# Optimization experiments

Measured on AMD Instinct MI355X. Metric: run time of the kernel, lower is better.

Reference implementation:

```python
import jax, jax.numpy as jnp
import numpy as np

B, NF, HS, S = 4, 5, 512, 1024  # batch, face strips, face side dims (L=9, S=2*HS)


def _wrap_prev(region, x, j, i, w, rev=False):
    # neighbour on previous face strip, wrapping face 0 -> face 4
    vm = x[:, :4, j, i]
    vw = x[:, 4, j, i]
    if rev:
        vm = jnp.flip(vm, -1)
        vw = jnp.flip(vw, -1)
    return jnp.concatenate([(vw - region[:, 0])[:, None] * w,
                            (vm - region[:, 1:]) * w], axis=1)


def _wrap_next(region, x, j, i, w, rev=False):
    # neighbour on next face strip, wrapping face 4 -> face 0
    vm = x[:, 1:, j, i]
    vw = x[:, 0, j, i]
    if rev:
        vm = jnp.flip(vm, -1)
        vw = jnp.flip(vw, -1)
    return jnp.concatenate([(vm - region[:, :4]) * w,
                            (vw - region[:, 4])[:, None] * w], axis=1)


def _gradient(x, poles, wi, we, wcn, wne, wnne, wnw, wnww, wwe, wsw, wsse, wse, wcs):
    Bx, Fx, HS, S = x.shape
    out = jnp.zeros((Bx, 4, Fx, HS, S), x.dtype)

    def put(o, rows, cols, comps):
        return o.at[:, :, :, rows, cols].set(jnp.stack(comps, axis=1))

    # inner grid
    ii = x[:, :, 1:HS-1, 1:S-1]
    comps = [
        (x[:, :, :HS-2, :S-2] - ii) * wi[0],
        (x[:, :, 2:HS, 2:S] - ii) * wi[1],
        (x[:, :, :HS-2, 1:S-1] - ii) * wi[2] + (x[:, :, 1:HS-1, 2:S] - ii) * wi[3],
        (x[:, :, 1:HS-1, :S-2] - ii) * wi[4] + (x[:, :, 2:HS, 1:S-1] - ii) * wi[5],
    ]
    out = put(out, slice(1, HS-1), slice(1, S-1), comps)

    # east edge
    ei = x[:, :, 0, 1:HS]
    comps = [
        _wrap_prev(ei, x, HS-1, slice(HS, S-1), we[0]),
        (x[:, :, 1, 2:HS+1] - ei) * we[1],
        _wrap_prev(ei, x, HS-1, slice(HS+1, S), we[2]) + (x[:, :, 0, 2:HS+1] - ei) * we[3],
        (x[:, :, 0, 0:HS-1] - ei) * we[4] + (x[:, :, 1, 1:HS] - ei) * we[5],
    ]
    out = put(out, 0, slice(1, HS), comps)

    # cn corner
    ci = x[:, :, 0, HS]
    comps = [
        _wrap_prev(ci, x, HS-1, S-1, wcn[0]),
        (x[:, :, 1, HS+1] - ci) * wcn[1],
        (x[:, :, 0, HS+1] - ci) * wcn[2],
        (x[:, :, 0, HS-1] - ci) * wcn[3] + (x[:, :, 1, HS] - ci) * wcn[4],
    ]
    out = put(out, 0, HS, comps)

    # ne edge
    ni = x[:, :, 0, HS+1:S-1]
    comps = [
        _wrap_prev(ni, x, slice(1, HS-1), S-1, wne[0], rev=True) + _wrap_prev(ni, x, slice(2, HS), S-1, wne[1], rev=True),
        (x[:, :, 1, HS+2:S] - ni) * wne[2] + (x[:, :, 1, HS+1:S-1] - ni) * wne[3],
        (x[:, :, 0, HS+2:S] - ni) * wne[4],
        (x[:, :, 0, HS:S-2] - ni) * wne[5],
    ]
    out = put(out, 0, slice(HS+1, S-1), comps)

    # nne corner (north pole neighbour)
    qi = x[:, :, 0, S-1]
    comps = [
        _wrap_prev(qi, x, 0, S-1, wnne[0]) + _wrap_prev(qi, x, 1, S-1, wnne[1]),
        _wrap_next(qi, x, 0, S-1, wnne[2]) + (x[:, :, 1, S-1] - qi) * wnne[3],
        (poles[:, 1] - qi) * wnne[4],
        (x[:, :, 0, S-2] - qi) * wnne[5],
    ]
    out = put(out, 0, S-1, comps)

    # nw edge
    vi = x[:, :, 1:HS-1, S-1]
    comps = [
        (x[:, :, 0:HS-2, S-2] - vi) * wnw[0],
        _wrap_next(vi, x, 0, slice(HS+1, S-1), wnw[1], rev=True),
        (x[:, :, 0:HS-2, S-1] - vi) * wnw[2] + _wrap_next(vi, x, 0, slice(HS+2, S), wnw[3], rev=True),
        (x[:, :, 1:HS-1, S-2] - vi) * wnw[4] + (x[:, :, 2:HS, S-1] - vi) * wnw[5],
    ]
    out = put(out, slice(1, HS-1), S-1, comps)

    # nww corner
    gi = x[:, :, HS-1, S-1]
    comps = [
        (x[:, :, HS-2, S-2] - gi) * wnww[0],
        _wrap_next(gi, x, 0, HS, wnww[1]),
        (x[:, :, HS-2, S-1] - gi) * wnww[2] + _wrap_next(gi, x, 0, HS+1, wnww[3]),
        (x[:, :, HS-1, S-2] - gi) * wnww[4] + _wrap_next(gi, x, 0, HS-1, wnww[5]),
    ]
    out = put(out, HS-1, S-1, comps)

    # west edge
    ui = x[:, :, HS-1, HS:S-1]
    comps = [
        (x[:, :, HS-2, HS-1:S-2] - ui) * wwe[0],
        _wrap_next(ui, x, 0, slice(1, HS), wwe[1]),
        (x[:, :, HS-2, HS:S-1] - ui) * wwe[2] + (x[:, :, HS-1, HS+1:S] - ui) * wwe[3],
        (x[:, :, HS-1, HS-1:S-2] - ui) * wwe[4] + _wrap_next(ui, x, 0, slice(0, HS-1), wwe[5]),
    ]
    out = put(out, HS-1, slice(HS, S-1), comps)

    # sw edge
    si = x[:, :, HS-1, 1:HS]
    comps = [
        (x[:, :, HS-2, 0:HS-1] - si) * wsw[0],
        _wrap_next(si, x, slice(0, HS-1), 0, wsw[1], rev=True),
        (x[:, :, HS-2, 1:HS] - si) * wsw[2] + (x[:, :, HS-1, 2:HS+1] - si) * wsw[3],
        (x[:, :, HS-1, 0:HS-1] - si) * wsw[4] + _wrap_next(si, x, slice(1, HS), 0, wsw[5], rev=True),
    ]
    out = put(out, HS-1, slice(1, HS), comps)

    # sse corner (south pole neighbour)
    pi = x[:, :, HS-1, 0]
    comps = [
        _wrap_prev(pi, x, HS-1, 0, wsse[0]),
        _wrap_next(pi, x, HS-1, 0, wsse[1]),
        (x[:, :, HS-2, 0] - pi) * wsse[2] + (x[:, :, HS-1, 1] - pi) * wsse[3],
        (poles[:, 0] - pi) * wsse[4],
    ]
    out = put(out, HS-1, 0, comps)

    # se edge
    ri = x[:, :, 1:HS-1, 0]
    comps = [
        _wrap_prev(ri, x, HS-1, slice(2, HS), wse[0], rev=True) + _wrap_prev(ri, x, HS-1, slice(1, HS-1), wse[1], rev=True),
        (x[:, :, 1:HS-1, 1] - ri) * wse[2] + (x[:, :, 2:HS, 1] - ri) * wse[3],
        (x[:, :, 0:HS-2, 0] - ri) * wse[4],
        (x[:, :, 2:HS, 0] - ri) * wse[5],
    ]
    out = put(out, slice(1, HS-1), 0, comps)

    # cs corner
    di = x[:, :, 0, 0]
    comps = [
        _wrap_prev(di, x, HS-1, HS-1, wcs[0]),
        (x[:, :, 1, 1] - di) * wcs[1],
        _wrap_prev(di, x, HS-1, HS, wcs[2]) + (x[:, :, 0, 1] - di) * wcs[3],
        (x[:, :, 1, 0] - di) * wcs[4],
    ]
    out = put(out, 0, 0, comps)
    return out


def setup_inputs() -> dict:
    key = jax.random.key(0)
    ks = jax.random.split(key, 14)
    rn = lambda k, s: jax.random.normal(k, s, dtype=jnp.float32)
    return {
        "x": rn(ks[0], (B, NF, HS, S)),
        "poles": rn(ks[1], (B, 2, 1)),
        "w_inner": rn(ks[2], (6, HS-2, S-2)),
        "w_east": rn(ks[3], (6, HS-1)),
        "w_cn": rn(ks[4], (5,)),
        "w_ne": rn(ks[5], (6, HS-2)),
        "w_nne": rn(ks[6], (6,)),
        "w_nw": rn(ks[7], (6, HS-2)),
        "w_nww": rn(ks[8], (6,)),
        "w_west": rn(ks[9], (6, HS-1)),
        "w_sw": rn(ks[10], (6, HS-1)),
        "w_sse": rn(ks[11], (5,)),
        "w_se": rn(ks[12], (6, HS-2)),
        "w_cs": rn(ks[13], (5,)),
    }


def reference(x, poles, w_inner, w_east, w_cn, w_ne, w_nne, w_nw, w_nww, w_west, w_sw, w_sse, w_se, w_cs):
    # output: [B, 4, 5, HS, S] weighted neighbour-difference stencil components
    return _gradient(x, poles, w_inner, w_east, w_cn, w_ne, w_nne, w_nw, w_nww,
                     w_west, w_sw, w_sse, w_se, w_cs)
```

## Files before the change

kernel.cpp:

```cpp
#include <hip/hip_runtime.h>

#define Bc  4
#define NFc 5
#define HSc 512
#define Sc  1024
#define WSr (Sc - 2)
#define WSp ((HSc - 2) * WSr)

typedef float f4 __attribute__((ext_vector_type(4)));

static __device__ __forceinline__ f4 load4u(const float* p) {
    f4 r;
    __builtin_memcpy(&r, p, 16);
    return r;
}

static __device__ __forceinline__ void inner_scalar(
    const float* __restrict__ xf, const float* __restrict__ wi,
    int j, int i, float cc, float* c)
{
    const size_t wb = (size_t)(j - 1) * WSr + (i - 1);
    const float w0 = wi[wb];
    const float w1 = wi[wb + WSp];
    const float w2 = wi[wb + 2 * (size_t)WSp];
    const float w3 = wi[wb + 3 * (size_t)WSp];
    const float w4 = wi[wb + 4 * (size_t)WSp];
    const float w5 = wi[wb + 5 * (size_t)WSp];
    c[0] = (xf[(size_t)(j - 1) * Sc + (i - 1)] - cc) * w0;
    c[1] = (xf[(size_t)(j + 1) * Sc + (i + 1)] - cc) * w1;
    c[2] = (xf[(size_t)(j - 1) * Sc + i] - cc) * w2
         + (xf[(size_t)j * Sc + (i + 1)] - cc) * w3;
    c[3] = (xf[(size_t)j * Sc + (i - 1)] - cc) * w4
         + (xf[(size_t)(j + 1) * Sc + i] - cc) * w5;
}

__global__ __launch_bounds__(256) void icograd_bulk(
    const float* __restrict__ x, const float* __restrict__ wi,
    const float* __restrict__ wnw, const float* __restrict__ wse,
    float* __restrict__ out)
{
    const int t  = threadIdx.x;
    const int j  = blockIdx.x + 1;
    const int bf = blockIdx.y;
    const int b  = bf / NFc;
    const int f  = bf % NFc;

    const size_t xb = (size_t)b * (NFc * HSc * Sc);
    const float* xf = x + xb + (size_t)f * (HSc * Sc);
    const float* rm = xf + (size_t)(j - 1) * Sc;
    const float* rc = xf + (size_t)j * Sc;
    const float* rp = xf + (size_t)(j + 1) * Sc;
    const int i0 = t * 4;

    float c0[4], c1[4], c2[4], c3[4];

    if (t >= 1 && t <= 254) {
        const f4 xm = *(const f4*)(rm + i0);
        const f4 xc = *(const f4*)(rc + i0);
        const f4 xp = *(const f4*)(rp + i0);
        const float xml = rm[i0 - 1];
        const float xcl = rc[i0 - 1];
        const float xcr = rc[i0 + 4];
        const float xpr = rp[i0 + 4];

        const float* wrow = wi + (size_t)(j - 1) * WSr + (i0 - 1);
        const f4 w0 = load4u(wrow);
        const f4 w1 = load4u(wrow + (size_t)WSp);
        const f4 w2 = load4u(wrow + 2 * (size_t)WSp);
        const f4 w3 = load4u(wrow + 3 * (size_t)WSp);
        const f4 w4 = load4u(wrow + 4 * (size_t)WSp);
        const f4 w5 = load4u(wrow + 5 * (size_t)WSp);

        const float am1[4] = {xml, xm.x, xm.y, xm.z};
        const float acm[4] = {xcl, xc.x, xc.y, xc.z};
        const float acp[4] = {xc.y, xc.z, xc.w, xcr};
        const float app[4] = {xp.y, xp.z, xp.w, xpr};
        const float xcv[4] = {xc.x, xc.y, xc.z, xc.w};
        const float xmv[4] = {xm.x, xm.y, xm.z, xm.w};
        const float xpv[4] = {xp.x, xp.y, xp.z, xp.w};
        const float w0v[4] = {w0.x, w0.y, w0.z, w0.w};
        const float w1v[4] = {w1.x, w1.y, w1.z, w1.w};
        const float w2v[4] = {w2.x, w2.y, w2.z, w2.w};
        const float w3v[4] = {w3.x, w3.y, w3.z, w3.w};
        const float w4v[4] = {w4.x, w4.y, w4.z, w4.w};
        const float w5v[4] = {w5.x, w5.y, w5.z, w5.w};

#pragma unroll
        for (int e = 0; e < 4; ++e) {
            const float cc = xcv[e];
            c0[e] = (am1[e] - cc) * w0v[e];
            c1[e] = (app[e] - cc) * w1v[e];
            c2[e] = (xmv[e] - cc) * w2v[e] + (acp[e] - cc) * w3v[e];
            c3[e] = (acm[e] - cc) * w4v[e] + (xpv[e] - cc) * w5v[e];
        }
    } else if (t == 0) {
        {
            const int m = j - 1;
            const int fp = (f == 0) ? 4 : f - 1;
            const float* xq = x + xb + (size_t)fp * (HSc * Sc);
            const float cc = rc[0];
            float cw[4];
            cw[0] = (xq[(size_t)(HSc - 1) * Sc + (511 - m)] - cc) * wse[0 * 510 + m]
                  + (xq[(size_t)(HSc - 1) * Sc + (510 - m)] - cc) * wse[1 * 510 + m];
            cw[1] = (rc[1] - cc) * wse[2 * 510 + m]
                  + (rp[1] - cc) * wse[3 * 510 + m];
            cw[2] = (rm[0] - cc) * wse[4 * 510 + m];
            cw[3] = (rp[0] - cc) * wse[5 * 510 + m];
            c0[0] = cw[0]; c1[0] = cw[1]; c2[0] = cw[2]; c3[0] = cw[3];
        }
#pragma unroll
        for (int e = 1; e < 4; ++e) {
            float cw[4];
            inner_scalar(xf, wi, j, e, rc[e], cw);
            c0[e] = cw[0]; c1[e] = cw[1]; c2[e] = cw[2]; c3[e] = cw[3];
        }
    } else {
#pragma unroll
        for (int e = 0; e < 3; ++e) {
            const int i = 1020 + e;
            float cw[4];
            inner_scalar(xf, wi, j, i, rc[i], cw);
            c0[e] = cw[0]; c1[e] = cw[1]; c2[e] = cw[2]; c3[e] = cw[3];
        }
        {
            const int m = j - 1;
            const int fn = (f == 4) ? 0 : f + 1;
            const float* xq = x + xb + (size_t)fn * (HSc * Sc);
            const float cc = rc[Sc - 1];
            float cw[4];
            cw[0] = (rm[Sc - 2] - cc) * wnw[0 * 510 + m];
            cw[1] = (xq[Sc - 2 - m] - cc) * wnw[1 * 510 + m];
            cw[2] = (rm[Sc - 1] - cc) * wnw[2 * 510 + m]
                  + (xq[Sc - 1 - m] - cc) * wnw[3 * 510 + m];
            cw[3] = (rc[Sc - 2] - cc) * wnw[4 * 510 + m]
                  + (rp[Sc - 1] - cc) * wnw[5 * 510 + m];
            c0[3] = cw[0]; c1[3] = cw[1]; c2[3] = cw[2]; c3[3] = cw[3];
        }
    }

    const size_t cs = (size_t)NFc * HSc * Sc;
    float* ob = out + ((size_t)b * (4 * NFc) + f) * (HSc * Sc)
                    + (size_t)j * Sc + i0;
    f4 o0 = {c0[0], c0[1], c0[2], c0[3]};
    f4 o1 = {c1[0], c1[1], c1[2], c1[3]};
    f4 o2 = {c2[0], c2[1], c2[2], c2[3]};
    f4 o3 = {c3[0], c3[1], c3[2], c3[3]};
    *(f4*)(ob)          = o0;
    *(f4*)(ob + cs)     = o1;
    *(f4*)(ob + 2 * cs) = o2;
    *(f4*)(ob + 3 * cs) = o3;
}

#define X(ff,jj,ii) x[xb + ((size_t)(ff)*HSc + (size_t)(jj))*Sc + (size_t)(ii)]
#define LW(arr,k,stride,m) (arr)[(k)*(stride)+(m)]

__global__ __launch_bounds__(256) void icograd_edge(
    const float* __restrict__ x,    const float* __restrict__ poles,
    const float* __restrict__ we,   const float* __restrict__ wcn,
    const float* __restrict__ wne,  const float* __restrict__ wnne,
    const float* __restrict__ wnww, const float* __restrict__ wwe,
    const float* __restrict__ wsw,  const float* __restrict__ wsse,
    const float* __restrict__ wcs,  float* __restrict__ out)
{
    const int i  = blockIdx.x * blockDim.x + threadIdx.x;
    const int j  = blockIdx.y ? (HSc - 1) : 0;
    const int bf = blockIdx.z;
    const int b  = bf / NFc;
    const int f  = bf % NFc;

    const size_t xb = (size_t)b * (NFc * HSc * Sc);
    const float  cc = X(f, j, i);
    const int fp = (f == 0) ? 4 : f - 1;
    const int fn = (f == 4) ? 0 : f + 1;

    float c0, c1, c2, c3;

    if (j == 0) {
        if (i == 0) {
            c0 = (X(fp, HSc - 1, HSc - 1) - cc) * wcs[0];
            c1 = (X(f, 1, 1) - cc) * wcs[1];
            c2 = (X(fp, HSc - 1, HSc) - cc) * wcs[2] + (X(f, 0, 1) - cc) * wcs[3];
            c3 = (X(f, 1, 0) - cc) * wcs[4];
        } else if (i <= HSc - 1) {
            const int m = i - 1;
            c0 = (X(fp, HSc - 1, HSc + m) - cc) * LW(we, 0, 511, m);
            c1 = (X(f, 1, i + 1) - cc) * LW(we, 1, 511, m);
            c2 = (X(fp, HSc - 1, HSc + 1 + m) - cc) * LW(we, 2, 511, m)
               + (X(f, 0, i + 1) - cc) * LW(we, 3, 511, m);
            c3 = (X(f, 0, i - 1) - cc) * LW(we, 4, 511, m)
               + (X(f, 1, i)     - cc) * LW(we, 5, 511, m);
        } else if (i == HSc) {
            c0 = (X(fp, HSc - 1, Sc - 1) - cc) * wcn[0];
            c1 = (X(f, 1, HSc + 1) - cc) * wcn[1];
            c2 = (X(f, 0, HSc + 1) - cc) * wcn[2];
            c3 = (X(f, 0, HSc - 1) - cc) * wcn[3] + (X(f, 1, HSc) - cc) * wcn[4];
        } else if (i < Sc - 1) {
            const int m = i - (HSc + 1);
            c0 = (X(fp, 510 - m, Sc - 1) - cc) * LW(wne, 0, 510, m)
               + (X(fp, 511 - m, Sc - 1) - cc) * LW(wne, 1, 510, m);
            c1 = (X(f, 1, i + 1) - cc) * LW(wne, 2, 510, m)
               + (X(f, 1, i)     - cc) * LW(wne, 3, 510, m);
            c2 = (X(f, 0, i + 1) - cc) * LW(wne, 4, 510, m);
            c3 = (X(f, 0, i - 1) - cc) * LW(wne, 5, 510, m);
        } else {
            const float p1 = poles[b * 2 + 1];
            c0 = (X(fp, 0, Sc - 1) - cc) * wnne[0]
               + (X(fp, 1, Sc - 1) - cc) * wnne[1];
            c1 = (X(fn, 0, Sc - 1) - cc) * wnne[2]
               + (X(f,  1, Sc - 1) - cc) * wnne[3];
            c2 = (p1 - cc) * wnne[4];
            c3 = (X(f, 0, Sc - 2) - cc) * wnne[5];
        }
    } else {
        if (i == 0) {
            const float p0 = poles[b * 2 + 0];
            c0 = (X(fp, HSc - 1, 0) - cc) * wsse[0];
            c1 = (X(fn, HSc - 1, 0) - cc) * wsse[1];
            c2 = (X(f, HSc - 2, 0) - cc) * wsse[2]
               + (X(f, HSc - 1, 1) - cc) * wsse[3];
            c3 = (p0 - cc) * wsse[4];
        } else if (i <= HSc - 1) {
            const int m = i - 1;
            c0 = (X(f, HSc - 2, i - 1) - cc) * LW(wsw, 0, 511, m);
            c1 = (X(fn, 510 - m, 0) - cc) * LW(wsw, 1, 511, m);
            c2 = (X(f, HSc - 2, i)     - cc) * LW(wsw, 2, 511, m)
               + (X(f, HSc - 1, i + 1) - cc) * LW(wsw, 3, 511, m);
            c3 = (X(f, HSc - 1, i - 1) - cc) * LW(wsw, 4, 511, m)
               + (X(fn, 511 - m, 0)    - cc) * LW(wsw, 5, 511, m);
        } else if (i < Sc - 1) {
            const int m = i - HSc;
            c0 = (X(f, HSc - 2, i - 1) - cc) * LW(wwe, 0, 511, m);
            c1 = (X(fn, 0, 1 + m) - cc) * LW(wwe, 1, 511, m);
            c2 = (X(f, HSc - 2, i)     - cc) * LW(wwe, 2, 511, m)
               + (X(f, HSc - 1, i + 1) - cc) * LW(wwe, 3, 511, m);
            c3 = (X(f, HSc - 1, i - 1) - cc) * LW(wwe, 4, 511, m)
               + (X(fn, 0, m)          - cc) * LW(wwe, 5, 511, m);
        } else {
            c0 = (X(f, HSc - 2, Sc - 2) - cc) * wnww[0];
            c1 = (X(fn, 0, HSc) - cc) * wnww[1];
            c2 = (X(f, HSc - 2, Sc - 1) - cc) * wnww[2]
               + (X(fn, 0, HSc + 1)     - cc) * wnww[3];
            c3 = (X(f, HSc - 1, Sc - 2) - cc) * wnww[4]
               + (X(fn, 0, HSc - 1)     - cc) * wnww[5];
        }
    }

    const size_t cs = (size_t)NFc * HSc * Sc;
    const size_t ob = ((size_t)b * (4 * NFc) + f) * (HSc * Sc)
                    + (size_t)j * Sc + (size_t)i;
    out[ob]          = c0;
    out[ob + cs]     = c1;
    out[ob + 2 * cs] = c2;
    out[ob + 3 * cs] = c3;
}

extern "C" void kernel_launch(void* const* d_in, const int* in_sizes, int n_in,
                              void* d_out, int out_size, void* d_ws, size_t ws_size,
                              hipStream_t stream) {
    const float* x    = (const float*)d_in[0];
    const float* pl   = (const float*)d_in[1];
    const float* wi   = (const float*)d_in[2];
    const float* we   = (const float*)d_in[3];
    const float* wcn  = (const float*)d_in[4];
    const float* wne  = (const float*)d_in[5];
    const float* wnne = (const float*)d_in[6];
    const float* wnw  = (const float*)d_in[7];
    const float* wnww = (const float*)d_in[8];
    const float* wwe  = (const float*)d_in[9];
    const float* wsw  = (const float*)d_in[10];
    const float* wsse = (const float*)d_in[11];
    const float* wse  = (const float*)d_in[12];
    const float* wcs  = (const float*)d_in[13];
    float* out = (float*)d_out;

    icograd_bulk<<<dim3(HSc - 2, Bc * NFc, 1), dim3(256, 1, 1), 0, stream>>>(
        x, wi, wnw, wse, out);
    icograd_edge<<<dim3(Sc / 256, 2, Bc * NFc), dim3(256, 1, 1), 0, stream>>>(
        x, pl, we, wcn, wne, wnne, wnww, wwe, wsw, wsse, wcs, out);
}
```

Baseline: 262.1 us.

## Fuse bulk and edge kernels, loop faces per block to reuse weights

Merges the interior and boundary kernels into a single launch, with 8 extra blocks per batch handling the two edge rows. Each block now iterates over all five face strips, so per-position weights are loaded once into registers and reused five times instead of being re-read per face. This cuts weight traffic and one launch, but shrinks the grid and serialises face work within each thread, reducing memory-level parallelism.

```diff
diff --git a/kernel.cpp b/kernel.cpp
--- a/kernel.cpp
+++ b/kernel.cpp
@@ -6,6 +6,7 @@
 #define Sc  1024
 #define WSr (Sc - 2)
 #define WSp ((HSc - 2) * WSr)
+#define PS  (HSc * Sc)
 
 typedef float f4 __attribute__((ext_vector_type(4)));
 
@@ -15,243 +16,339 @@
     return r;
 }
 
-static __device__ __forceinline__ void inner_scalar(
-    const float* __restrict__ xf, const float* __restrict__ wi,
-    int j, int i, float cc, float* c)
-{
-    const size_t wb = (size_t)(j - 1) * WSr + (i - 1);
-    const float w0 = wi[wb];
-    const float w1 = wi[wb + WSp];
-    const float w2 = wi[wb + 2 * (size_t)WSp];
-    const float w3 = wi[wb + 3 * (size_t)WSp];
-    const float w4 = wi[wb + 4 * (size_t)WSp];
-    const float w5 = wi[wb + 5 * (size_t)WSp];
-    c[0] = (xf[(size_t)(j - 1) * Sc + (i - 1)] - cc) * w0;
-    c[1] = (xf[(size_t)(j + 1) * Sc + (i + 1)] - cc) * w1;
-    c[2] = (xf[(size_t)(j - 1) * Sc + i] - cc) * w2
-         + (xf[(size_t)j * Sc + (i + 1)] - cc) * w3;
-    c[3] = (xf[(size_t)j * Sc + (i - 1)] - cc) * w4
-         + (xf[(size_t)(j + 1) * Sc + i] - cc) * w5;
-}
-
-__global__ __launch_bounds__(256) void icograd_bulk(
-    const float* __restrict__ x, const float* __restrict__ wi,
-    const float* __restrict__ wnw, const float* __restrict__ wse,
+#define X(ff,jj,ii) x[xb + ((size_t)(ff) * HSc + (size_t)(jj)) * Sc + (size_t)(ii)]
+
+__global__ __launch_bounds__(256) void icograd_fused(
+    const float* __restrict__ x,    const float* __restrict__ poles,
+    const float* __restrict__ wi,   const float* __restrict__ we,
+    const float* __restrict__ wcn,  const float* __restrict__ wne,
+    const float* __restrict__ wnne, const float* __restrict__ wnw,
+    const float* __restrict__ wnww, const float* __restrict__ wwe,
+    const float* __restrict__ wsw,  const float* __restrict__ wsse,
+    const float* __restrict__ wse,  const float* __restrict__ wcs,
     float* __restrict__ out)
 {
-    const int t  = threadIdx.x;
-    const int j  = blockIdx.x + 1;
-    const int bf = blockIdx.y;
-    const int b  = bf / NFc;
-    const int f  = bf % NFc;
-
-    const size_t xb = (size_t)b * (NFc * HSc * Sc);
-    const float* xf = x + xb + (size_t)f * (HSc * Sc);
-    const float* rm = xf + (size_t)(j - 1) * Sc;
-    const float* rc = xf + (size_t)j * Sc;
-    const float* rp = xf + (size_t)(j + 1) * Sc;
-    const int i0 = t * 4;
-
-    float c0[4], c1[4], c2[4], c3[4];
-
-    if (t >= 1 && t <= 254) {
-        const f4 xm = *(const f4*)(rm + i0);
-        const f4 xc = *(const f4*)(rc + i0);
-        const f4 xp = *(const f4*)(rp + i0);
-        const float xml = rm[i0 - 1];
-        const float xcl = rc[i0 - 1];
-        const float xcr = rc[i0 + 4];
-        const float xpr = rp[i0 + 4];
-
-        const float* wrow = wi + (size_t)(j - 1) * WSr + (i0 - 1);
-        const f4 w0 = load4u(wrow);
-        const f4 w1 = load4u(wrow + (size_t)WSp);
-        const f4 w2 = load4u(wrow + 2 * (size_t)WSp);
-        const f4 w3 = load4u(wrow + 3 * (size_t)WSp);
-        const f4 w4 = load4u(wrow + 4 * (size_t)WSp);
-        const f4 w5 = load4u(wrow + 5 * (size_t)WSp);
-
-        const float am1[4] = {xml, xm.x, xm.y, xm.z};
-        const float acm[4] = {xcl, xc.x, xc.y, xc.z};
-        const float acp[4] = {xc.y, xc.z, xc.w, xcr};
-        const float app[4] = {xp.y, xp.z, xp.w, xpr};
-        const float xcv[4] = {xc.x, xc.y, xc.z, xc.w};
-        const float xmv[4] = {xm.x, xm.y, xm.z, xm.w};
-        const float xpv[4] = {xp.x, xp.y, xp.z, xp.w};
-        const float w0v[4] = {w0.x, w0.y, w0.z, w0.w};
-        const float w1v[4] = {w1.x, w1.y, w1.z, w1.w};
-        const float w2v[4] = {w2.x, w2.y, w2.z, w2.w};
-        const float w3v[4] = {w3.x, w3.y, w3.z, w3.w};
-        const float w4v[4] = {w4.x, w4.y, w4.z, w4.w};
-        const float w5v[4] = {w5.x, w5.y, w5.z, w5.w};
-
-#pragma unroll
-        for (int e = 0; e < 4; ++e) {
-            const float cc = xcv[e];
-            c0[e] = (am1[e] - cc) * w0v[e];
-            c1[e] = (app[e] - cc) * w1v[e];
-            c2[e] = (xmv[e] - cc) * w2v[e] + (acp[e] - cc) * w3v[e];
-            c3[e] = (acm[e] - cc) * w4v[e] + (xpv[e] - cc) * w5v[e];
+    const int t = threadIdx.x;
+    const int b = blockIdx.y;
+
+    const size_t xb  = (size_t)b * (NFc * PS);
+    const size_t cs  = (size_t)NFc * PS;
+    const size_t obB = (size_t)b * (4 * NFc) * PS;
+
+    if (blockIdx.x >= 8) {
+        const int j  = blockIdx.x - 7;
+        const int m  = j - 1;
+        const int i0 = t * 4;
+
+        if (t >= 1 && t <= 254) {
+            const float* wrow = wi + (size_t)m * WSr + (i0 - 1);
+            const f4 w0 = load4u(wrow);
+            const f4 w1 = load4u(wrow + (size_t)WSp);
+            const f4 w2 = load4u(wrow + 2 * (size_t)WSp);
+            const f4 w3 = load4u(wrow + 3 * (size_t)WSp);
+            const f4 w4 = load4u(wrow + 4 * (size_t)WSp);
+            const f4 w5 = load4u(wrow + 5 * (size_t)WSp);
+            const float w0v[4] = {w0.x, w0.y, w0.z, w0.w};
+            const float w1v[4] = {w1.x, w1.y, w1.z, w1.w};
+            const float w2v[4] = {w2.x, w2.y, w2.z, w2.w};
+            const float w3v[4] = {w3.x, w3.y, w3.z, w3.w};
+            const float w4v[4] = {w4.x, w4.y, w4.z, w4.w};
+            const float w5v[4] = {w5.x, w5.y, w5.z, w5.w};
+
+            const float* xf  = x + xb;
+            float*       ob0 = out + obB + (size_t)j * Sc + i0;
+
+            for (int f = 0; f < NFc; ++f, xf += PS, ob0 += PS) {
+                const float* rm = xf + (size_t)(j - 1) * Sc;
+                const float* rc = xf + (size_t)j * Sc;
+                const float* rp = xf + (size_t)(j + 1) * Sc;
+
+                const f4 xm = *(const f4*)(rm + i0);
+                const f4 xc = *(const f4*)(rc + i0);
+                const f4 xp = *(const f4*)(rp + i0);
+                const float xml = rm[i0 - 1];
+                const float xcl = rc[i0 - 1];
+                const float xcr = rc[i0 + 4];
+                const float xpr = rp[i0 + 4];
+
+                const float am1[4] = {xml, xm.x, xm.y, xm.z};
+                const float acm[4] = {xcl, xc.x, xc.y, xc.z};
+                const float acp[4] = {xc.y, xc.z, xc.w, xcr};
+                const float app[4] = {xp.y, xp.z, xp.w, xpr};
+                const float xcv[4] = {xc.x, xc.y, xc.z, xc.w};
+                const float xmv[4] = {xm.x, xm.y, xm.z, xm.w};
+                const float xpv[4] = {xp.x, xp.y, xp.z, xp.w};
+
+                float c0[4], c1[4], c2[4], c3[4];
+#pragma unroll
+                for (int e = 0; e < 4; ++e) {
+                    const float cc = xcv[e];
+                    c0[e] = (am1[e] - cc) * w0v[e];
+                    c1[e] = (app[e] - cc) * w1v[e];
+                    c2[e] = (xmv[e] - cc) * w2v[e] + (acp[e] - cc) * w3v[e];
+                    c3[e] = (acm[e] - cc) * w4v[e] + (xpv[e] - cc) * w5v[e];
+                }
+
+                f4 o0 = {c0[0], c0[1], c0[2], c0[3]};
+                f4 o1 = {c1[0], c1[1], c1[2], c1[3]};
+                f4 o2 = {c2[0], c2[1], c2[2], c2[3]};
+                f4 o3 = {c3[0], c3[1], c3[2], c3[3]};
+                *(f4*)(ob0)          = o0;
+                *(f4*)(ob0 + cs)     = o1;
+                *(f4*)(ob0 + 2 * cs) = o2;
+                *(f4*)(ob0 + 3 * cs) = o3;
+            }
+        } else if (t == 0) {
+            const float s0 = wse[0 * 510 + m], s1 = wse[1 * 510 + m];
+            const float s2 = wse[2 * 510 + m], s3 = wse[3 * 510 + m];
+            const float s4 = wse[4 * 510 + m], s5 = wse[5 * 510 + m];
+            float wv[6][3];
+#pragma unroll
+            for (int k = 0; k < 6; ++k)
+#pragma unroll
+                for (int e = 0; e < 3; ++e)
+                    wv[k][e] = wi[(size_t)k * WSp + (size_t)m * WSr + e];
+
+            const float* xf  = x + xb;
+            float*       ob0 = out + obB + (size_t)j * Sc;
+
+            for (int f = 0; f < NFc; ++f, xf += PS, ob0 += PS) {
+                const int fp = (f == 0) ? 4 : f - 1;
+                const float* xq = x + xb + (size_t)fp * PS + (size_t)(HSc - 1) * Sc;
+                const float* rm = xf + (size_t)(j - 1) * Sc;
+                const float* rc = xf + (size_t)j * Sc;
+                const float* rp = xf + (size_t)(j + 1) * Sc;
+
+                float c0[4], c1[4], c2[4], c3[4];
+                {
+                    const float cc = rc[0];
+                    c0[0] = (xq[511 - m] - cc) * s0 + (xq[510 - m] - cc) * s1;
+                    c1[0] = (rc[1] - cc) * s2 + (rp[1] - cc) * s3;
+                    c2[0] = (rm[0] - cc) * s4;
+                    c3[0] = (rp[0] - cc) * s5;
+                }
+#pragma unroll
+                for (int e = 1; e < 4; ++e) {
+                    const float cc = rc[e];
+                    c0[e] = (rm[e - 1] - cc) * wv[0][e - 1];
+                    c1[e] = (rp[e + 1] - cc) * wv[1][e - 1];
+                    c2[e] = (rm[e] - cc) * wv[2][e - 1] + (rc[e + 1] - cc) * wv[3][e - 1];
+                    c3[e] = (rc[e - 1] - cc) * wv[4][e - 1] + (rp[e] - cc) * wv[5][e - 1];
+                }
+
+                f4 o0 = {c0[0], c0[1], c0[2], c0[3]};
+                f4 o1 = {c1[0], c1[1], c1[2], c1[3]};
+                f4 o2 = {c2[0], c2[1], c2[2], c2[3]};
+                f4 o3 = {c3[0], c3[1], c3[2], c3[3]};
+                *(f4*)(ob0)          = o0;
+                *(f4*)(ob0 + cs)     = o1;
+                *(f4*)(ob0 + 2 * cs) = o2;
+                *(f4*)(ob0 + 3 * cs) = o3;
+            }
+        } else {
+            const float n0 = wnw[0 * 510 + m], n1 = wnw[1 * 510 + m];
+            const float n2 = wnw[2 * 510 + m], n3 = wnw[3 * 510 + m];
+            const float n4 = wnw[4 * 510 + m], n5 = wnw[5 * 510 + m];
+            float wv[6][3];
+#pragma unroll
+            for (int k = 0; k < 6; ++k)
+#pragma unroll
+                for (int e = 0; e < 3; ++e)
+                    wv[k][e] = wi[(size_t)k * WSp + (size_t)m * WSr + (1019 + e)];
+
+            const float* xf  = x + xb;
+            float*       ob0 = out + obB + (size_t)j * Sc + 1020;
+
+            for (int f = 0; f < NFc; ++f, xf += PS, ob0 += PS) {
+                const int fn = (f == 4) ? 0 : f + 1;
+                const float* xq = x + xb + (size_t)fn * PS;
+                const float* rm = xf + (size_t)(j - 1) * Sc;
+                const float* rc = xf + (size_t)j * Sc;
+                const float* rp = xf + (size_t)(j + 1) * Sc;
+
+                float c0[4], c1[4], c2[4], c3[4];
+#pragma unroll
+                for (int e = 0; e < 3; ++e) {
+                    const int i = 1020 + e;
+                    const float cc = rc[i];
+                    c0[e] = (rm[i - 1] - cc) * wv[0][e];
+                    c1[e] = (rp[i + 1] - cc) * wv[1][e];
+                    c2[e] = (rm[i] - cc) * wv[2][e] + (rc[i + 1] - cc) * wv[3][e];
+                    c3[e] = (rc[i - 1] - cc) * wv[4][e] + (rp[i] - cc) * wv[5][e];
+                }
+                {
+                    const float cc = rc[Sc - 1];
+                    c0[3] = (rm[Sc - 2] - cc) * n0;
+                    c1[3] = (xq[1022 - m] - cc) * n1;
+                    c2[3] = (rm[Sc - 1] - cc) * n2 + (xq[1023 - m] - cc) * n3;
+                    c3[3] = (rc[Sc - 2] - cc) * n4 + (rp[Sc - 1] - cc) * n5;
+                }
+
+                f4 o0 = {c0[0], c0[1], c0[2], c0[3]};
+                f4 o1 = {c1[0], c1[1], c1[2], c1[3]};
+                f4 o2 = {c2[0], c2[1], c2[2], c2[3]};
+                f4 o3 = {c3[0], c3[1], c3[2], c3[3]};
+                *(f4*)(ob0)          = o0;
+                *(f4*)(ob0 + cs)     = o1;
+                *(f4*)(ob0 + 2 * cs) = o2;
+                *(f4*)(ob0 + 3 * cs) = o3;
+            }
         }
-    } else if (t == 0) {
-        {
-            const int m = j - 1;
-            const int fp = (f == 0) ? 4 : f - 1;
-            const float* xq = x + xb + (size_t)fp * (HSc * Sc);
-            const float cc = rc[0];
-            float cw[4];
-            cw[0] = (xq[(size_t)(HSc - 1) * Sc + (511 - m)] - cc) * wse[0 * 510 + m]
-                  + (xq[(size_t)(HSc - 1) * Sc + (510 - m)] - cc) * wse[1 * 510 + m];
-            cw[1] = (rc[1] - cc) * wse[2 * 510 + m]
-                  + (rp[1] - cc) * wse[3 * 510 + m];
-            cw[2] = (rm[0] - cc) * wse[4 * 510 + m];
-            cw[3] = (rp[0] - cc) * wse[5 * 510 + m];
-            c0[0] = cw[0]; c1[0] = cw[1]; c2[0] = cw[2]; c3[0] = cw[3];
+        return;
+    }
+
+    {
+        const int e8 = blockIdx.x;
+        const int j  = (e8 < 4) ? 0 : (HSc - 1);
+        const int i  = (e8 & 3) * 256 + t;
+        const size_t obRow = obB + (size_t)j * Sc + (size_t)i;
+
+#define STORE4(ff) do {                                              \
+        const size_t _o = obRow + (size_t)(ff) * PS;                 \
+        out[_o]          = c0;                                       \
+        out[_o + cs]     = c1;                                       \
+        out[_o + 2 * cs] = c2;                                       \
+        out[_o + 3 * cs] = c3;                                       \
+    } while (0)
+
+        if (j == 0) {
+            if (i == 0) {
+                const float a0 = wcs[0], a1 = wcs[1], a2 = wcs[2], a3 = wcs[3], a4 = wcs[4];
+                for (int f = 0; f < NFc; ++f) {
+                    const int fp = (f == 0) ? 4 : f - 1;
+                    const float cc = X(f, 0, 0);
+                    float c0 = (X(fp, HSc - 1, HSc - 1) - cc) * a0;
+                    float c1 = (X(f, 1, 1) - cc) * a1;
+                    float c2 = (X(fp, HSc - 1, HSc) - cc) * a2 + (X(f, 0, 1) - cc) * a3;
+                    float c3 = (X(f, 1, 0) - cc) * a4;
+                    STORE4(f);
+                }
+            } else if (i <= HSc - 1) {
+                const int m = i - 1;
+                const float a0 = we[0 * 511 + m], a1 = we[1 * 511 + m];
+                const float a2 = we[2 * 511 + m], a3 = we[3 * 511 + m];
+                const float a4 = we[4 * 511 + m], a5 = we[5 * 511 + m];
+                for (int f = 0; f < NFc; ++f) {
+                    const int fp = (f == 0) ? 4 : f - 1;
+                    const float cc = X(f, 0, i);
+                    float c0 = (X(fp, HSc - 1, HSc + m) - cc) * a0;
+                    float c1 = (X(f, 1, i + 1) - cc) * a1;
+                    float c2 = (X(fp, HSc - 1, HSc + 1 + m) - cc) * a2
+                             + (X(f, 0, i + 1) - cc) * a3;
+                    float c3 = (X(f, 0, i - 1) - cc) * a4
+                             + (X(f, 1, i)     - cc) * a5;
+                    STORE4(f);
+                }
+            } else if (i == HSc) {
+                const float a0 = wcn[0], a1 = wcn[1], a2 = wcn[2], a3 = wcn[3], a4 = wcn[4];
+                for (int f = 0; f < NFc; ++f) {
+                    const int fp = (f == 0) ? 4 : f - 1;
+                    const float cc = X(f, 0, HSc);
+                    float c0 = (X(fp, HSc - 1, Sc - 1) - cc) * a0;
+                    float c1 = (X(f, 1, HSc + 1) - cc) * a1;
+                    float c2 = (X(f, 0, HSc + 1) - cc) * a2;
+                    float c3 = (X(f, 0, HSc - 1) - cc) * a3 + (X(f, 1, HSc) - cc) * a4;
+                    STORE4(f);
+                }
+            } else if (i < Sc - 1) {
+                const int m = i - (HSc + 1);
+                const float a0 = wne[0 * 510 + m], a1 = wne[1 * 510 + m];
+                const float a2 = wne[2 * 510 + m], a3 = wne[3 * 510 + m];
+                const float a4 = wne[4 * 510 + m], a5 = wne[5 * 510 + m];
+                for (int f = 0; f < NFc; ++f) {
+                    const int fp = (f == 0) ? 4 : f - 1;
+                    const float cc = X(f, 0, i);
+                    float c0 = (X(fp, 510 - m, Sc - 1) - cc) * a0
+                             + (X(fp, 511 - m, Sc - 1) - cc) * a1;
+                    float c1 = (X(f, 1, i + 1) - cc) * a2
+                             + (X(f, 1, i)     - cc) * a3;
+                    float c2 = (X(f, 0, i + 1) - cc) * a4;
+                    float c3 = (X(f, 0, i - 1) - cc) * a5;
+                    STORE4(f);
+                }
+            } else {
+                const float p1 = poles[b * 2 + 1];
+                const float a0 = wnne[0], a1 = wnne[1], a2 = wnne[2];
+                const float a3 = wnne[3], a4 = wnne[4], a5 = wnne[5];
+                for (int f = 0; f < NFc; ++f) {
+                    const int fp = (f == 0) ? 4 : f - 1;
+                    const int fn = (f == 4) ? 0 : f + 1;
+                    const float cc = X(f, 0, Sc - 1);
+                    float c0 = (X(fp, 0, Sc - 1) - cc) * a0
+                             + (X(fp, 1, Sc - 1) - cc) * a1;
+                    float c1 = (X(fn, 0, Sc - 1) - cc) * a2
+                             + (X(f,  1, Sc - 1) - cc) * a3;
+                    float c2 = (p1 - cc) * a4;
+                    float c3 = (X(f, 0, Sc - 2) - cc) * a5;
+                    STORE4(f);
+                }
+            }
+        } else {
+            if (i == 0) {
+                const float p0 = poles[b * 2 + 0];
+                const float a0 = wsse[0], a1 = wsse[1], a2 = wsse[2];
+                const float a3 = wsse[3], a4 = wsse[4];
+                for (int f = 0; f < NFc; ++f) {
+                    const int fp = (f == 0) ? 4 : f - 1;
+                    const int fn = (f == 4) ? 0 : f + 1;
+                    const float cc = X(f, HSc - 1, 0);
+                    float c0 = (X(fp, HSc - 1, 0) - cc) * a0;
+                    float c1 = (X(fn, HSc - 1, 0) - cc) * a1;
+                    float c2 = (X(f, HSc - 2, 0) - cc) * a2
+                             + (X(f, HSc - 1, 1) - cc) * a3;
+                    float c3 = (p0 - cc) * a4;
+                    STORE4(f);
+                }
+            } else if (i <= HSc - 1) {
+                const int m = i - 1;
+                const float a0 = wsw[0 * 511 + m], a1 = wsw[1 * 511 + m];
+                const float a2 = wsw[2 * 511 + m], a3 = wsw[3 * 511 + m];
+                const float a4 = wsw[4 * 511 + m], a5 = wsw[5 * 511 + m];
+                for (int f = 0; f < NFc; ++f) {
+                    const int fn = (f == 4) ? 0 : f + 1;
+                    const float cc = X(f, HSc - 1, i);
+                    float c0 = (X(f, HSc - 2, i - 1) - cc) * a0;
+                    float c1 = (X(fn, 510 - m, 0) - cc) * a1;
+                    float c2 = (X(f, HSc - 2, i)     - cc) * a2
+                             + (X(f, HSc - 1, i + 1) - cc) * a3;
+                    float c3 = (X(f, HSc - 1, i - 1) - cc) * a4
+                             + (X(fn, 511 - m, 0)    - cc) * a5;
+                    STORE4(f);
+                }
+            } else if (i < Sc - 1) {
+                const int m = i - HSc;
+                const float a0 = wwe[0 * 511 + m], a1 = wwe[1 * 511 + m];
+                const float a2 = wwe[2 * 511 + m], a3 = wwe[3 * 511 + m];
+                const float a4 = wwe[4 * 511 + m], a5 = wwe[5 * 511 + m];
+                for (int f = 0; f < NFc; ++f) {
+                    const int fn = (f == 4) ? 0 : f + 1;
+                    const float cc = X(f, HSc - 1, i);
+                    float c0 = (X(f, HSc - 2, i - 1) - cc) * a0;
+                    float c1 = (X(fn, 0, 1 + m) - cc) * a1;
+                    float c2 = (X(f, HSc - 2, i)     - cc) * a2
+                             + (X(f, HSc - 1, i + 1) - cc) * a3;
+                    float c3 = (X(f, HSc - 1, i - 1) - cc) * a4
+                             + (X(fn, 0, m)          - cc) * a5;
+                    STORE4(f);
+                }
+            } else {
+                const float a0 = wnww[0], a1 = wnww[1], a2 = wnww[2];
+                const float a3 = wnww[3], a4 = wnww[4], a5 = wnww[5];
+                for (int f = 0; f < NFc; ++f) {
+                    const int fn = (f == 4) ? 0 : f + 1;
+                    const float cc = X(f, HSc - 1, Sc - 1);
+                    float c0 = (X(f, HSc - 2, Sc - 2) - cc) * a0;
+                    float c1 = (X(fn, 0, HSc) - cc) * a1;
+                    float c2 = (X(f, HSc - 2, Sc - 1) - cc) * a2
+                             + (X(fn, 0, HSc + 1)     - cc) * a3;
+                    float c3 = (X(f, HSc - 1, Sc - 2) - cc) * a4
+                             + (X(fn, 0, HSc - 1)     - cc) * a5;
+                    STORE4(f);
+                }
+            }
         }
-#pragma unroll
-        for (int e = 1; e < 4; ++e) {
-            float cw[4];
-            inner_scalar(xf, wi, j, e, rc[e], cw);
-            c0[e] = cw[0]; c1[e] = cw[1]; c2[e] = cw[2]; c3[e] = cw[3];
-        }
-    } else {
-#pragma unroll
-        for (int e = 0; e < 3; ++e) {
-            const int i = 1020 + e;
-            float cw[4];
-            inner_scalar(xf, wi, j, i, rc[i], cw);
-            c0[e] = cw[0]; c1[e] = cw[1]; c2[e] = cw[2]; c3[e] = cw[3];
-        }
-        {
-            const int m = j - 1;
-            const int fn = (f == 4) ? 0 : f + 1;
-            const float* xq = x + xb + (size_t)fn * (HSc * Sc);
-            const float cc = rc[Sc - 1];
-            float cw[4];
-            cw[0] = (rm[Sc - 2] - cc) * wnw[0 * 510 + m];
-            cw[1] = (xq[Sc - 2 - m] - cc) * wnw[1 * 510 + m];
-            cw[2] = (rm[Sc - 1] - cc) * wnw[2 * 510 + m]
-                  + (xq[Sc - 1 - m] - cc) * wnw[3 * 510 + m];
-            cw[3] = (rc[Sc - 2] - cc) * wnw[4 * 510 + m]
-                  + (rp[Sc - 1] - cc) * wnw[5 * 510 + m];
-            c0[3] = cw[0]; c1[3] = cw[1]; c2[3] = cw[2]; c3[3] = cw[3];
-        }
+#undef STORE4
     }
-
-    const size_t cs = (size_t)NFc * HSc * Sc;
-    float* ob = out + ((size_t)b * (4 * NFc) + f) * (HSc * Sc)
-                    + (size_t)j * Sc + i0;
-    f4 o0 = {c0[0], c0[1], c0[2], c0[3]};
-    f4 o1 = {c1[0], c1[1], c1[2], c1[3]};
-    f4 o2 = {c2[0], c2[1], c2[2], c2[3]};
-    f4 o3 = {c3[0], c3[1], c3[2], c3[3]};
-    *(f4*)(ob)          = o0;
-    *(f4*)(ob + cs)     = o1;
-    *(f4*)(ob + 2 * cs) = o2;
-    *(f4*)(ob + 3 * cs) = o3;
-}
-
-#define X(ff,jj,ii) x[xb + ((size_t)(ff)*HSc + (size_t)(jj))*Sc + (size_t)(ii)]
-#define LW(arr,k,stride,m) (arr)[(k)*(stride)+(m)]
-
-__global__ __launch_bounds__(256) void icograd_edge(
-    const float* __restrict__ x,    const float* __restrict__ poles,
-    const float* __restrict__ we,   const float* __restrict__ wcn,
-    const float* __restrict__ wne,  const float* __restrict__ wnne,
-    const float* __restrict__ wnww, const float* __restrict__ wwe,
-    const float* __restrict__ wsw,  const float* __restrict__ wsse,
-    const float* __restrict__ wcs,  float* __restrict__ out)
-{
-    const int i  = blockIdx.x * blockDim.x + threadIdx.x;
-    const int j  = blockIdx.y ? (HSc - 1) : 0;
-    const int bf = blockIdx.z;
-    const int b  = bf / NFc;
-    const int f  = bf % NFc;
-
-    const size_t xb = (size_t)b * (NFc * HSc * Sc);
-    const float  cc = X(f, j, i);
-    const int fp = (f == 0) ? 4 : f - 1;
-    const int fn = (f == 4) ? 0 : f + 1;
-
-    float c0, c1, c2, c3;
-
-    if (j == 0) {
-        if (i == 0) {
-            c0 = (X(fp, HSc - 1, HSc - 1) - cc) * wcs[0];
-            c1 = (X(f, 1, 1) - cc) * wcs[1];
-            c2 = (X(fp, HSc - 1, HSc) - cc) * wcs[2] + (X(f, 0, 1) - cc) * wcs[3];
-            c3 = (X(f, 1, 0) - cc) * wcs[4];
-        } else if (i <= HSc - 1) {
-            const int m = i - 1;
-            c0 = (X(fp, HSc - 1, HSc + m) - cc) * LW(we, 0, 511, m);
-            c1 = (X(f, 1, i + 1) - cc) * LW(we, 1, 511, m);
-            c2 = (X(fp, HSc - 1, HSc + 1 + m) - cc) * LW(we, 2, 511, m)
-               + (X(f, 0, i + 1) - cc) * LW(we, 3, 511, m);
-            c3 = (X(f, 0, i - 1) - cc) * LW(we, 4, 511, m)
-               + (X(f, 1, i)     - cc) * LW(we, 5, 511, m);
-        } else if (i == HSc) {
-            c0 = (X(fp, HSc - 1, Sc - 1) - cc) * wcn[0];
-            c1 = (X(f, 1, HSc + 1) - cc) * wcn[1];
-            c2 = (X(f, 0, HSc + 1) - cc) * wcn[2];
-            c3 = (X(f, 0, HSc - 1) - cc) * wcn[3] + (X(f, 1, HSc) - cc) * wcn[4];
-        } else if (i < Sc - 1) {
-            const int m = i - (HSc + 1);
-            c0 = (X(fp, 510 - m, Sc - 1) - cc) * LW(wne, 0, 510, m)
-               + (X(fp, 511 - m, Sc - 1) - cc) * LW(wne, 1, 510, m);
-            c1 = (X(f, 1, i + 1) - cc) * LW(wne, 2, 510, m)
-               + (X(f, 1, i)     - cc) * LW(wne, 3, 510, m);
-            c2 = (X(f, 0, i + 1) - cc) * LW(wne, 4, 510, m);
-            c3 = (X(f, 0, i - 1) - cc) * LW(wne, 5, 510, m);
-        } else {
-            const float p1 = poles[b * 2 + 1];
-            c0 = (X(fp, 0, Sc - 1) - cc) * wnne[0]
-               + (X(fp, 1, Sc - 1) - cc) * wnne[1];
-            c1 = (X(fn, 0, Sc - 1) - cc) * wnne[2]
-               + (X(f,  1, Sc - 1) - cc) * wnne[3];
-            c2 = (p1 - cc) * wnne[4];
-            c3 = (X(f, 0, Sc - 2) - cc) * wnne[5];
-        }
-    } else {
-        if (i == 0) {
-            const float p0 = poles[b * 2 + 0];
-            c0 = (X(fp, HSc - 1, 0) - cc) * wsse[0];
-            c1 = (X(fn, HSc - 1, 0) - cc) * wsse[1];
-            c2 = (X(f, HSc - 2, 0) - cc) * wsse[2]
-               + (X(f, HSc - 1, 1) - cc) * wsse[3];
-            c3 = (p0 - cc) * wsse[4];
-        } else if (i <= HSc - 1) {
-            const int m = i - 1;
-            c0 = (X(f, HSc - 2, i - 1) - cc) * LW(wsw, 0, 511, m);
-            c1 = (X(fn, 510 - m, 0) - cc) * LW(wsw, 1, 511, m);
-            c2 = (X(f, HSc - 2, i)     - cc) * LW(wsw, 2, 511, m)
-               + (X(f, HSc - 1, i + 1) - cc) * LW(wsw, 3, 511, m);
-            c3 = (X(f, HSc - 1, i - 1) - cc) * LW(wsw, 4, 511, m)
-               + (X(fn, 511 - m, 0)    - cc) * LW(wsw, 5, 511, m);
-        } else if (i < Sc - 1) {
-            const int m = i - HSc;
-            c0 = (X(f, HSc - 2, i - 1) - cc) * LW(wwe, 0, 511, m);
-            c1 = (X(fn, 0, 1 + m) - cc) * LW(wwe, 1, 511, m);
-            c2 = (X(f, HSc - 2, i)     - cc) * LW(wwe, 2, 511, m)
-               + (X(f, HSc - 1, i + 1) - cc) * LW(wwe, 3, 511, m);
-            c3 = (X(f, HSc - 1, i - 1) - cc) * LW(wwe, 4, 511, m)
-               + (X(fn, 0, m)          - cc) * LW(wwe, 5, 511, m);
-        } else {
-            c0 = (X(f, HSc - 2, Sc - 2) - cc) * wnww[0];
-            c1 = (X(fn, 0, HSc) - cc) * wnww[1];
-            c2 = (X(f, HSc - 2, Sc - 1) - cc) * wnww[2]
-               + (X(fn, 0, HSc + 1)     - cc) * wnww[3];
-            c3 = (X(f, HSc - 1, Sc - 2) - cc) * wnww[4]
-               + (X(fn, 0, HSc - 1)     - cc) * wnww[5];
-        }
-    }
-
-    const size_t cs = (size_t)NFc * HSc * Sc;
-    const size_t ob = ((size_t)b * (4 * NFc) + f) * (HSc * Sc)
-                    + (size_t)j * Sc + (size_t)i;
-    out[ob]          = c0;
-    out[ob + cs]     = c1;
-    out[ob + 2 * cs] = c2;
-    out[ob + 3 * cs] = c3;
 }
 
 extern "C" void kernel_launch(void* const* d_in, const int* in_sizes, int n_in,
@@ -273,8 +370,6 @@
     const float* wcs  = (const float*)d_in[13];
     float* out = (float*)d_out;
 
-    icograd_bulk<<<dim3(HSc - 2, Bc * NFc, 1), dim3(256, 1, 1), 0, stream>>>(
-        x, wi, wnw, wse, out);
-    icograd_edge<<<dim3(Sc / 256, 2, Bc * NFc), dim3(256, 1, 1), 0, stream>>>(
-        x, pl, we, wcn, wne, wnne, wnww, wwe, wsw, wsse, wcs, out);
+    icograd_fused<<<dim3(8 + (HSc - 2), Bc, 1), dim3(256, 1, 1), 0, stream>>>(
+        x, pl, wi, we, wcn, wne, wnne, wnw, wnww, wwe, wsw, wsse, wse, wcs, out);
 }
```

After: 263.8 us. Within noise of the previous version (+0.7%).
